# Kernel optimization log

Measured on AMD Instinct MI355X. Metric: run time of the kernel, lower is better.

## Reference

```python
import jax, jax.numpy as jnp
import numpy as np

N = 50000
E = 800000
D_IN = 128
D_OUT = 128


def setup_inputs() -> dict:
    key = jax.random.key(0)
    ks = jax.random.split(key, 10)
    features = jax.random.normal(ks[0], (N, D_IN), dtype=jnp.float32)
    edge_index = jax.random.randint(ks[1], (2, E), 0, N, dtype=jnp.int64)
    s = 1.0 / np.sqrt(D_IN)
    W1 = jax.random.uniform(ks[2], (D_OUT, D_IN), jnp.float32, -s, s)
    b1 = jax.random.uniform(ks[3], (D_OUT,), jnp.float32, -s, s)
    W2 = jax.random.uniform(ks[4], (D_OUT, D_IN), jnp.float32, -s, s)
    b2 = jax.random.uniform(ks[5], (D_OUT,), jnp.float32, -s, s)
    so = 1.0 / np.sqrt(D_OUT)
    wa1 = jax.random.uniform(ks[6], (D_OUT,), jnp.float32, -so, so)
    ba1 = jax.random.uniform(ks[7], (), jnp.float32, -so, so)
    wa2 = jax.random.uniform(ks[8], (D_OUT,), jnp.float32, -so, so)
    ba2 = jax.random.uniform(ks[9], (), jnp.float32, -so, so)
    return {"features": features, "W1": W1, "b1": b1, "W2": W2, "b2": b2,
            "wa1": wa1, "ba1": ba1, "wa2": wa2, "ba2": ba2,
            "edge_index": edge_index}


def reference(features, W1, b1, W2, b2, wa1, ba1, wa2, ba2, edge_index):
    n = features.shape[0]
    fi = jax.nn.relu(features @ W1.T + b1)  # [n, d_out]
    fj = jax.nn.relu(features @ W2.T + b2)  # [n, d_out]
    a1 = fi @ wa1 + ba1  # [n]
    a2 = fj @ wa2 + ba2  # [n]
    # append self-loops, as in the torch code
    self_idx = jnp.arange(n, dtype=edge_index.dtype)
    rows = jnp.concatenate([edge_index[0], self_idx])
    cols = jnp.concatenate([edge_index[1], self_idx])
    # per-edge attention: sigmoid(a1[i] + a2[j]) == dense sigmoid(a1 + a2.T)[i, j]
    att = jax.nn.sigmoid(a1[rows] + a2[cols])  # [E + n]
    msgs = att[:, None] * fj[cols]  # [E + n, d_out]
    agg = jax.ops.segment_sum(msgs, rows, num_segments=n)  # duplicates sum, like sparse.mm
    return agg + fi
```

## Files before the change

kernel.cpp:

```cpp
#include <hip/hip_runtime.h>
#include <hip/hip_bf16.h>

#define DD 128
#define PCHUNK 8192
#define ACAP 2048

typedef __bf16 bf16x8 __attribute__((ext_vector_type(8)));
typedef unsigned short u16x8 __attribute__((ext_vector_type(8)));
typedef float f32x4 __attribute__((ext_vector_type(4)));

__device__ __forceinline__ float lo16(unsigned int d) {
    union { unsigned int i; float f; } v; v.i = d << 16; return v.f;
}
__device__ __forceinline__ float hi16(unsigned int d) {
    union { unsigned int i; float f; } v; v.i = d & 0xffff0000u; return v.f;
}
__device__ __forceinline__ unsigned short f2bf(float f) {
    union { float f; unsigned int i; } v; v.f = f;
    unsigned int x = v.i;
    return (unsigned short)((x + 0x7fffu + ((x >> 16) & 1u)) >> 16);
}
__device__ __forceinline__ float fsig(float x) {
    return __builtin_amdgcn_rcpf(1.f + __expf(-x));
}

__global__ __launch_bounds__(256)
void gat_prolog(const unsigned int* __restrict__ EI, int* __restrict__ flags,
                int* __restrict__ binCnt,
                const float* __restrict__ W1, const float* __restrict__ W2,
                unsigned int* __restrict__ wbf)
{
    const int t = threadIdx.x;
    if (t < 64) {
        const int vote_i64 = (EI[2 * t + 1] == 0u) ? 1 : 0;
        unsigned long long mi = __ballot(vote_i64);
        if (t == 0) flags[1] = (__popcll(mi) == 64) ? 1 : 0;
    }
#pragma unroll
    for (int i = 0; i < 4; ++i) binCnt[t + 256 * i] = 0;
#pragma unroll
    for (int i = 0; i < 32; ++i) {
        const int g = i * 256 + t;
        const float4 v = (g < 4096) ? ((const float4*)W1)[g]
                                    : ((const float4*)W2)[g - 4096];
        uint2 p;
        p.x = ((unsigned)f2bf(v.y) << 16) | f2bf(v.x);
        p.y = ((unsigned)f2bf(v.w) << 16) | f2bf(v.z);
        ((uint2*)wbf)[g] = p;
    }
}

__global__ __launch_bounds__(256)
void gat_gemm_mfma(const float* __restrict__ X,
                   const unsigned short* __restrict__ wbf,
                   const float* __restrict__ b1, const float* __restrict__ b2,
                   const float* __restrict__ wa1, const float* __restrict__ ba1,
                   const float* __restrict__ wa2, const float* __restrict__ ba2,
                   float* __restrict__ out, unsigned int* __restrict__ fjb,
                   float* __restrict__ a1g, float* __restrict__ a2g, int N)
{
    const int t = threadIdx.x, wave = t >> 6, lane = t & 63;
    const int quad = lane >> 4, l15 = lane & 15;
    const int rowbase = blockIdx.x * 64;

    __shared__ unsigned short At[64 * 136];
    __shared__ float fjL[64 * 132];
    __shared__ float parts[4][64];
    __shared__ float attL[64];

    const float bab1 = *ba1, bab2 = *ba2;

    bf16x8 bf[4][4];
    float biasv[4], attwv[4];
#pragma unroll
    for (int ct = 0; ct < 4; ++ct) {
        const int n = wave * 64 + ct * 16 + l15;
        const unsigned short* wr = wbf + (size_t)n * 128;
        biasv[ct] = (n < 128) ? b1[n] : b2[n - 128];
        attwv[ct] = (n < 128) ? wa1[n] : wa2[n - 128];
#pragma unroll
        for (int ks = 0; ks < 4; ++ks)
            bf[ct][ks] = *(const bf16x8*)(wr + ks * 32 + quad * 8);
    }

    {
        const int r = t >> 2, q = t & 3;
        const int grow = rowbase + r;
#pragma unroll
        for (int i = 0; i < 8; ++i) {
            const int c = q * 32 + i * 4;
            float4 xv = make_float4(0.f, 0.f, 0.f, 0.f);
            if (grow < N) xv = *(const float4*)(X + (size_t)grow * DD + c);
            uint2 p;
            p.x = ((unsigned)f2bf(xv.y) << 16) | f2bf(xv.x);
            p.y = ((unsigned)f2bf(xv.w) << 16) | f2bf(xv.z);
            *(uint2*)&At[r * 136 + c] = p;
        }
    }
    __syncthreads();

    f32x4 acc[4][4];
#pragma unroll
    for (int rt = 0; rt < 4; ++rt)
#pragma unroll
        for (int ct = 0; ct < 4; ++ct)
            acc[rt][ct] = (f32x4){0.f, 0.f, 0.f, 0.f};

#pragma unroll
    for (int ks = 0; ks < 4; ++ks) {
#pragma unroll
        for (int rt = 0; rt < 4; ++rt) {
            const bf16x8 af = *(const bf16x8*)&At[(rt * 16 + l15) * 136 + ks * 32 + quad * 8];
#pragma unroll
            for (int ct = 0; ct < 4; ++ct)
                acc[rt][ct] = __builtin_amdgcn_mfma_f32_16x16x32_bf16(af, bf[ct][ks], acc[rt][ct], 0, 0, 0);
        }
    }

#pragma unroll
    for (int rt = 0; rt < 4; ++rt)
#pragma unroll
        for (int ct = 0; ct < 4; ++ct)
#pragma unroll
            for (int reg = 0; reg < 4; ++reg) {
                float v = acc[rt][ct][reg] + biasv[ct];
                acc[rt][ct][reg] = v > 0.f ? v : 0.f;
            }

    if (wave >= 2) {
#pragma unroll
        for (int rt = 0; rt < 4; ++rt)
#pragma unroll
            for (int ct = 0; ct < 4; ++ct)
#pragma unroll
                for (int reg = 0; reg < 4; ++reg) {
                    const int row = rt * 16 + quad * 4 + reg;
                    const int col = (wave - 2) * 64 + ct * 16 + l15;
                    fjL[row * 132 + col] = acc[rt][ct][reg];
                }
    }

#pragma unroll
    for (int rt = 0; rt < 4; ++rt) {
#pragma unroll
        for (int reg = 0; reg < 4; ++reg) {
            float p = acc[rt][0][reg] * attwv[0] + acc[rt][1][reg] * attwv[1]
                    + acc[rt][2][reg] * attwv[2] + acc[rt][3][reg] * attwv[3];
            p += __shfl_xor(p, 1);
            p += __shfl_xor(p, 2);
            p += __shfl_xor(p, 4);
            p += __shfl_xor(p, 8);
            if (l15 == 0) parts[wave][rt * 16 + quad * 4 + reg] = p;
        }
    }
    __syncthreads();

    if (t < 64) {
        const float A1 = parts[0][t] + parts[1][t] + bab1;
        const float A2 = parts[2][t] + parts[3][t] + bab2;
        attL[t] = 1.f / (1.f + expf(-(A1 + A2)));
        const int grow = rowbase + t;
        if (grow < N) { a1g[grow] = A1; a2g[grow] = A2; }
    }
    __syncthreads();

    if (wave < 2) {
#pragma unroll
        for (int rt = 0; rt < 4; ++rt)
#pragma unroll
            for (int ct = 0; ct < 4; ++ct)
#pragma unroll
                for (int reg = 0; reg < 4; ++reg) {
                    const int row = rt * 16 + quad * 4 + reg;
                    const int col = wave * 64 + ct * 16 + l15;
                    const int grow = rowbase + row;
                    if (grow < N)
                        out[(size_t)grow * DD + col] =
                            acc[rt][ct][reg] + attL[row] * fjL[row * 132 + col];
                }
    } else {
#pragma unroll 4
        for (int i = 0; i < 32; ++i) {
            const int idx = (wave - 2) * 2048 + i * 64 + lane;
            const int row = idx >> 6, d = idx & 63;
            const int grow = rowbase + row;
            if (grow < N) {
                const float lo = fjL[row * 132 + 2 * d];
                const float hi = fjL[row * 132 + 2 * d + 1];
                fjb[(size_t)grow * 64 + d] = ((unsigned)f2bf(hi) << 16) | f2bf(lo);
            }
        }
    }
}

__global__ __launch_bounds__(256)
void gat_part(const int* __restrict__ ei, int* __restrict__ binCnt,
              unsigned int* __restrict__ binned,
              int nEdges, int N, int NBINS, const int* __restrict__ flags)
{
    __shared__ int locHist[1024];
    __shared__ int locBase[1024];
    const int t = threadIdx.x;
    const int i64 = flags[1];
    const int base = blockIdx.x * PCHUNK;

    for (int i = t; i < NBINS; i += 256) locHist[i] = 0;
    __syncthreads();

    unsigned pk[32];
    short bn[32];
#pragma unroll
    for (int j = 0; j < 32; ++j) {
        const int e = base + j * 256 + t;
        if (e < nEdges) {
            int r = i64 ? ei[2 * e]            : ei[e];
            int c = i64 ? ei[2 * (nEdges + e)] : ei[nEdges + e];
            if ((unsigned)r >= (unsigned)N) r = 0;
            if ((unsigned)c >= (unsigned)N) c = 0;
            const int b = r >> 6;
            atomicAdd(&locHist[b], 1);
            pk[j] = ((unsigned)(r & 63) << 17) | (unsigned)c;
            bn[j] = (short)b;
        } else bn[j] = -1;
    }
    __syncthreads();
    for (int i = t; i < NBINS; i += 256) {
        const int c = locHist[i];
        locBase[i] = c ? atomicAdd(&binCnt[i], c) : 0;
    }
    __syncthreads();
    for (int i = t; i < NBINS; i += 256) locHist[i] = 0;
    __syncthreads();

#pragma unroll 2
    for (int j = 0; j < 32; ++j) {
        if (bn[j] >= 0) {
            const int b = bn[j];
            const int slot = locBase[b] + atomicAdd(&locHist[b], 1);
            if (slot < ACAP)
                binned[(size_t)b * ACAP + slot] = pk[j];
        }
    }
}

__global__ __launch_bounds__(256)
void gat_accum_bin(const int* __restrict__ binCnt, const unsigned int* __restrict__ binned,
                   const float* __restrict__ a1, const float* __restrict__ a2,
                   const unsigned int* __restrict__ fjb, float* __restrict__ out, int N)
{
    __shared__ unsigned short perm[ACAP];
    __shared__ int counts[32];
    __shared__ int rowStart[33];
    __shared__ int cursor[32];
    const int t = threadIdx.x, lane = t & 63, wave = t >> 6;
    const int b = blockIdx.x >> 1, half = blockIdx.x & 1;
    const int r0 = (b << 6) + (half << 5);
    const unsigned int* bp = binned + (size_t)b * ACAP;

    int cnt = binCnt[b];
    if (cnt > ACAP) cnt = ACAP;

    if (t < 32) counts[t] = 0;
    __syncthreads();
    for (int i = t; i < cnt; i += 256) {
        const int rl = bp[i] >> 17;
        if ((rl >> 5) == half) atomicAdd(&counts[rl & 31], 1);
    }
    __syncthreads();

    if (wave == 0 && lane < 32) {
        const int c0 = counts[lane];
        int s0 = c0;
#pragma unroll
        for (int off = 1; off < 32; off <<= 1) {
            const int o = __shfl_up(s0, off);
            if (lane >= off) s0 += o;
        }
        rowStart[lane] = s0 - c0;
        cursor[lane]   = s0 - c0;
        if (lane == 31) rowStart[32] = s0;
    }
    __syncthreads();
    for (int i = t; i < cnt; i += 256) {
        const int rl = bp[i] >> 17;
        if ((rl >> 5) == half)
            perm[atomicAdd(&cursor[rl & 31], 1)] = (unsigned short)i;
    }
    __syncthreads();

    for (int rl = wave; rl < 32; rl += 4) {
        const int row = r0 + rl;
        if (row >= N) break;
        const float a1r = a1[row];
        float2* op = (float2*)&out[(size_t)row * DD + 2 * lane];
        float2 cur = *op;
        const int s = rowStart[rl], eEnd = rowStart[rl + 1];
        float ax = 0.f, ay = 0.f;
        int e = s;
        for (; e + 8 <= eEnd; e += 8) {
            unsigned p[8];
#pragma unroll
            for (int j = 0; j < 8; ++j) p[j] = bp[perm[e + j]];
            unsigned d[8];
#pragma unroll
            for (int j = 0; j < 8; ++j) d[j] = fjb[(size_t)(p[j] & 0x1ffff) * 64 + lane];
            float av[8];
#pragma unroll
            for (int j = 0; j < 8; ++j) av[j] = a2[p[j] & 0x1ffff];
#pragma unroll
            for (int j = 0; j < 8; ++j) {
                const float att = fsig(a1r + av[j]);
                ax += att * lo16(d[j]);
                ay += att * hi16(d[j]);
            }
        }
        for (; e < eEnd; ++e) {
            const unsigned p = bp[perm[e]];
            const unsigned d = fjb[(size_t)(p & 0x1ffff) * 64 + lane];
            const float att = fsig(a1r + a2[p & 0x1ffff]);
            ax += att * lo16(d);
            ay += att * hi16(d);
        }
        cur.x += ax; cur.y += ay;
        *op = cur;
    }
}

extern "C" void kernel_launch(void* const* d_in, const int* in_sizes, int n_in,
                              void* d_out, int out_size, void* d_ws, size_t ws_size,
                              hipStream_t stream)
{
    const float* X   = (const float*)d_in[0];
    const float* W1  = (const float*)d_in[1];
    const float* b1  = (const float*)d_in[2];
    const float* W2  = (const float*)d_in[3];
    const float* b2  = (const float*)d_in[4];
    const float* wa1 = (const float*)d_in[5];
    const float* ba1 = (const float*)d_in[6];
    const float* wa2 = (const float*)d_in[7];
    const float* ba2 = (const float*)d_in[8];
    const int*   ei  = (const int*)d_in[9];

    const int N = in_sizes[0] / DD;
    const int E = in_sizes[9] / 2;
    const int NBINS = (N + 63) >> 6;

    int*   flags = (int*)d_ws;
    char*  base  = (char*)d_ws + 256;
    unsigned int* fjb    = (unsigned int*)base;
    unsigned int* binned = (unsigned int*)(base + (size_t)N * 64 * 4);
    float* a1     = (float*)((char*)binned + (size_t)NBINS * ACAP * 4);
    float* a2     = a1 + N;
    int*   binCnt = (int*)(a2 + N);
    unsigned int* wbf = (unsigned int*)(binCnt + 1024);

    gat_prolog<<<1, 256, 0, stream>>>((const unsigned int*)ei, flags, binCnt, W1, W2, wbf);

    gat_gemm_mfma<<<(N + 63) / 64, 256, 0, stream>>>(X, (const unsigned short*)wbf,
                                                     b1, b2, wa1, ba1, wa2, ba2,
                                                     (float*)d_out, fjb, a1, a2, N);

    gat_part<<<(E + PCHUNK - 1) / PCHUNK, 256, 0, stream>>>(ei, binCnt, binned,
                                                            E, N, NBINS, flags);

    gat_accum_bin<<<NBINS * 2, 256, 0, stream>>>(binCnt, binned, a1, a2, fjb,
                                                 (float*)d_out, N);
}
```

Baseline: 202.0 us.

## Merge edge partition and GEMM kernels into one launch with block-range dispatch

Combines the edge-binning kernel and the MFMA GEMM kernel into a single launch, where the first nPart blocks do edge partitioning and the remaining blocks do the feature GEMM. Each partition block now detects the index dtype itself instead of reading a flag from the prolog. The goal is to save one kernel launch and let the two independent phases run concurrently on the GPU. In exchange, both paths share one shared-memory allocation sized for the larger GEMM path, which may lower occupancy for the partition blocks.

```diff
diff --git a/kernel.cpp b/kernel.cpp
--- a/kernel.cpp
+++ b/kernel.cpp
@@ -6,7 +6,6 @@
 #define ACAP 2048
 
 typedef __bf16 bf16x8 __attribute__((ext_vector_type(8)));
-typedef unsigned short u16x8 __attribute__((ext_vector_type(8)));
 typedef float f32x4 __attribute__((ext_vector_type(4)));
 
 __device__ __forceinline__ float lo16(unsigned int d) {
@@ -25,17 +24,11 @@
 }
 
 __global__ __launch_bounds__(256)
-void gat_prolog(const unsigned int* __restrict__ EI, int* __restrict__ flags,
-                int* __restrict__ binCnt,
+void gat_prolog(int* __restrict__ binCnt,
                 const float* __restrict__ W1, const float* __restrict__ W2,
                 unsigned int* __restrict__ wbf)
 {
     const int t = threadIdx.x;
-    if (t < 64) {
-        const int vote_i64 = (EI[2 * t + 1] == 0u) ? 1 : 0;
-        unsigned long long mi = __ballot(vote_i64);
-        if (t == 0) flags[1] = (__popcll(mi) == 64) ? 1 : 0;
-    }
 #pragma unroll
     for (int i = 0; i < 4; ++i) binCnt[t + 256 * i] = 0;
 #pragma unroll
@@ -51,23 +44,78 @@
 }
 
 __global__ __launch_bounds__(256)
-void gat_gemm_mfma(const float* __restrict__ X,
-                   const unsigned short* __restrict__ wbf,
-                   const float* __restrict__ b1, const float* __restrict__ b2,
-                   const float* __restrict__ wa1, const float* __restrict__ ba1,
-                   const float* __restrict__ wa2, const float* __restrict__ ba2,
-                   float* __restrict__ out, unsigned int* __restrict__ fjb,
-                   float* __restrict__ a1g, float* __restrict__ a2g, int N)
+void gat_main(const float* __restrict__ X,
+              const unsigned short* __restrict__ wbf,
+              const float* __restrict__ b1, const float* __restrict__ b2,
+              const float* __restrict__ wa1, const float* __restrict__ ba1,
+              const float* __restrict__ wa2, const float* __restrict__ ba2,
+              float* __restrict__ out, unsigned int* __restrict__ fjb,
+              float* __restrict__ a1g, float* __restrict__ a2g,
+              const int* __restrict__ ei, int* __restrict__ binCnt,
+              unsigned int* __restrict__ binned,
+              int N, int nEdges, int NBINS, int nPart)
 {
+    __shared__ __align__(16) char smem[52480];
     const int t = threadIdx.x, wave = t >> 6, lane = t & 63;
+
+    if (blockIdx.x < nPart) {
+        int* locHist = (int*)smem;
+        int* locBase = (int*)(smem + 4096);
+        int* i64sh   = (int*)(smem + 8192);
+        const int base = blockIdx.x * PCHUNK;
+
+        if (t < 64) {
+            const int vote = (((const unsigned int*)ei)[2 * t + 1] == 0u) ? 1 : 0;
+            unsigned long long m = __ballot(vote);
+            if (t == 0) *i64sh = (__popcll(m) == 64) ? 1 : 0;
+        }
+        for (int i = t; i < NBINS; i += 256) locHist[i] = 0;
+        __syncthreads();
+        const int i64 = *i64sh;
+
+        unsigned pk[32];
+        short bn[32];
+#pragma unroll
+        for (int j = 0; j < 32; ++j) {
+            const int e = base + j * 256 + t;
+            if (e < nEdges) {
+                int r = i64 ? ei[2 * e]            : ei[e];
+                int c = i64 ? ei[2 * (nEdges + e)] : ei[nEdges + e];
+                if ((unsigned)r >= (unsigned)N) r = 0;
+                if ((unsigned)c >= (unsigned)N) c = 0;
+                const int b = r >> 6;
+                atomicAdd(&locHist[b], 1);
+                pk[j] = ((unsigned)(r & 63) << 17) | (unsigned)c;
+                bn[j] = (short)b;
+            } else bn[j] = -1;
+        }
+        __syncthreads();
+        for (int i = t; i < NBINS; i += 256) {
+            const int c = locHist[i];
+            locBase[i] = c ? atomicAdd(&binCnt[i], c) : 0;
+        }
+        __syncthreads();
+        for (int i = t; i < NBINS; i += 256) locHist[i] = 0;
+        __syncthreads();
+#pragma unroll 2
+        for (int j = 0; j < 32; ++j) {
+            if (bn[j] >= 0) {
+                const int b = bn[j];
+                const int slot = locBase[b] + atomicAdd(&locHist[b], 1);
+                if (slot < ACAP)
+                    binned[(size_t)b * ACAP + slot] = pk[j];
+            }
+        }
+        return;
+    }
+
+    unsigned short* At = (unsigned short*)smem;
+    float* fjL  = (float*)(smem + 17408);
+    float (*parts)[64] = (float(*)[64])(smem + 51200);
+    float* attL = (float*)(smem + 52224);
+
     const int quad = lane >> 4, l15 = lane & 15;
-    const int rowbase = blockIdx.x * 64;
-
-    __shared__ unsigned short At[64 * 136];
-    __shared__ float fjL[64 * 132];
-    __shared__ float parts[4][64];
-    __shared__ float attL[64];
-
+    const int rowbase = (blockIdx.x - nPart) * 64;
     const float bab1 = *ba1, bab2 = *ba2;
 
     bf16x8 bf[4][4];
@@ -194,56 +242,6 @@
 }
 
 __global__ __launch_bounds__(256)
-void gat_part(const int* __restrict__ ei, int* __restrict__ binCnt,
-              unsigned int* __restrict__ binned,
-              int nEdges, int N, int NBINS, const int* __restrict__ flags)
-{
-    __shared__ int locHist[1024];
-    __shared__ int locBase[1024];
-    const int t = threadIdx.x;
-    const int i64 = flags[1];
-    const int base = blockIdx.x * PCHUNK;
-
-    for (int i = t; i < NBINS; i += 256) locHist[i] = 0;
-    __syncthreads();
-
-    unsigned pk[32];
-    short bn[32];
-#pragma unroll
-    for (int j = 0; j < 32; ++j) {
-        const int e = base + j * 256 + t;
-        if (e < nEdges) {
-            int r = i64 ? ei[2 * e]            : ei[e];
-            int c = i64 ? ei[2 * (nEdges + e)] : ei[nEdges + e];
-            if ((unsigned)r >= (unsigned)N) r = 0;
-            if ((unsigned)c >= (unsigned)N) c = 0;
-            const int b = r >> 6;
-            atomicAdd(&locHist[b], 1);
-            pk[j] = ((unsigned)(r & 63) << 17) | (unsigned)c;
-            bn[j] = (short)b;
-        } else bn[j] = -1;
-    }
-    __syncthreads();
-    for (int i = t; i < NBINS; i += 256) {
-        const int c = locHist[i];
-        locBase[i] = c ? atomicAdd(&binCnt[i], c) : 0;
-    }
-    __syncthreads();
-    for (int i = t; i < NBINS; i += 256) locHist[i] = 0;
-    __syncthreads();
-
-#pragma unroll 2
-    for (int j = 0; j < 32; ++j) {
-        if (bn[j] >= 0) {
-            const int b = bn[j];
-            const int slot = locBase[b] + atomicAdd(&locHist[b], 1);
-            if (slot < ACAP)
-                binned[(size_t)b * ACAP + slot] = pk[j];
-        }
-    }
-}
-
-__global__ __launch_bounds__(256)
 void gat_accum_bin(const int* __restrict__ binCnt, const unsigned int* __restrict__ binned,
                    const float* __restrict__ a1, const float* __restrict__ a2,
                    const unsigned int* __restrict__ fjb, float* __restrict__ out, int N)
@@ -344,9 +342,10 @@
     const int N = in_sizes[0] / DD;
     const int E = in_sizes[9] / 2;
     const int NBINS = (N + 63) >> 6;
-
-    int*   flags = (int*)d_ws;
-    char*  base  = (char*)d_ws + 256;
+    const int nPart = (E + PCHUNK - 1) / PCHUNK;
+    const int nGemm = (N + 63) / 64;
+
+    char*  base  = (char*)d_ws;
     unsigned int* fjb    = (unsigned int*)base;
     unsigned int* binned = (unsigned int*)(base + (size_t)N * 64 * 4);
     float* a1     = (float*)((char*)binned + (size_t)NBINS * ACAP * 4);
@@ -354,14 +353,13 @@
     int*   binCnt = (int*)(a2 + N);
     unsigned int* wbf = (unsigned int*)(binCnt + 1024);
 
-    gat_prolog<<<1, 256, 0, stream>>>((const unsigned int*)ei, flags, binCnt, W1, W2, wbf);
-
-    gat_gemm_mfma<<<(N + 63) / 64, 256, 0, stream>>>(X, (const unsigned short*)wbf,
-                                                     b1, b2, wa1, ba1, wa2, ba2,
-                                                     (float*)d_out, fjb, a1, a2, N);
-
-    gat_part<<<(E + PCHUNK - 1) / PCHUNK, 256, 0, stream>>>(ei, binCnt, binned,
-                                                            E, N, NBINS, flags);
+    gat_prolog<<<1, 256, 0, stream>>>(binCnt, W1, W2, wbf);
+
+    gat_main<<<nPart + nGemm, 256, 0, stream>>>(X, (const unsigned short*)wbf,
+                                                b1, b2, wa1, ba1, wa2, ba2,
+                                                (float*)d_out, fjb, a1, a2,
+                                                ei, binCnt, binned,
+                                                N, E, NBINS, nPart);
 
     gat_accum_bin<<<NBINS * 2, 256, 0, stream>>>(binCnt, binned, a1, a2, fjb,
                                                  (float*)d_out, N);
```

Result: faster. 175.2 us (-13.3%).
